# Performance work log

Hardware: AMD Instinct MI355X
Metric: run time of the kernel (lower is better)

## Reference

```python
import jax, jax.numpy as jnp
import numpy as np

# Kornia's fixed 5x5 pyramid (binomial) kernel used by build_pyramid/pyrdown
_PYR_K = np.array([[1, 4, 6, 4, 1],
                   [4, 16, 24, 16, 4],
                   [6, 24, 36, 24, 6],
                   [4, 16, 24, 16, 4],
                   [1, 4, 6, 4, 1]], dtype=np.float32) / 256.0


def _pyrdown(x):
    """kornia pyrdown: 5x5 binomial blur (reflect pad) + bilinear resize to (H//2, W//2)."""
    B, C, H, W = x.shape
    xp = jnp.pad(x, ((0, 0), (0, 0), (2, 2), (2, 2)), mode='reflect')
    k = jnp.broadcast_to(jnp.asarray(_PYR_K, x.dtype), (C, 1, 5, 5))  # depthwise
    y = jax.lax.conv_general_dilated(
        xp, k, window_strides=(1, 1), padding='VALID',
        feature_group_count=C, dimension_numbers=('NCHW', 'OIHW', 'NCHW'))
    # torch F.interpolate bilinear align_corners=False == jax resize bilinear, antialias off
    return jax.image.resize(y, (B, C, H // 2, W // 2), method='bilinear', antialias=False)


def _norm_pc(x):
    """Per-channel min-max normalization to [0,1] over spatial dims."""
    mx = jnp.max(x, axis=(2, 3), keepdims=True)
    mn = jnp.min(x, axis=(2, 3), keepdims=True)
    return (x - mn) / (mx - mn)


def _avg_local_max(x):
    """Mean of 16x16 tile maxima; torch loop range(0, H-16, 16) skips the last tile
    row/col, and with zero tiles the torch code yields nan_to_num(0/0) == 0."""
    B, C, H, W = x.shape
    s = 16
    ny = len(range(0, H - s, s))
    nx = len(range(0, W - s, s))
    if ny == 0 or nx == 0:
        return jnp.zeros((B, C, 1, 1), x.dtype)
    t = x[:, :, :ny * s, :nx * s].reshape(B, C, ny, s, nx, s)
    lmax = jnp.max(t, axis=(3, 5))           # [B,C,ny,nx]
    return jnp.mean(lmax, axis=(2, 3)).reshape(B, C, 1, 1)


def _sm_normalization(x):
    d = _norm_pc(x)
    lm = _avg_local_max(d)
    return d * (1.0 - lm) ** 2


def setup_inputs() -> dict:
    key = jax.random.key(0)
    x = jax.random.normal(key, (8, 3, 512, 512), dtype=jnp.float32)
    return {"x": x}


def reference(x):
    B, C, H, W = x.shape
    inp = _norm_pc(x)
    max_level = int(H).bit_length() - 1   # 9 for H=512
    u = max_level - 1

    # Gaussian pyramid of length max_level: [inp, pyrdown(inp), ...]
    pyr = [inp]
    for _ in range(max_level - 1):
        pyr.append(_pyrdown(pyr[-1]))

    acc = None
    for i in range(u - 1):
        h, w = pyr[i + 1].shape[2], pyr[i + 1].shape[3]
        up = jnp.repeat(jnp.repeat(pyr[i + 2], 2, axis=2), 2, axis=3)[:, :, :h, :w]
        d = jnp.abs(pyr[i + 1] - up)
        nd = jax.image.resize(_sm_normalization(d), (B, C, H, W),
                              method='bilinear', antialias=False)
        acc = nd if acc is None else acc + nd

    return jnp.mean(acc, axis=1)  # [B,H,W]
```

## Files before the change

kernel.cpp:

```cpp
#include <hip/hip_runtime.h>
#include <math.h>

#define NPLANES 24
#define FINF 3.402823466e38f

__host__ __device__ __forceinline__ int d_off(int li) {
    return 2097152 - (2097152 >> (2 * li));
}

__device__ __forceinline__ int refl(int v, int S) {
    if (v < 0) v = -v;
    if (v >= S) v = 2 * S - 2 - v;
    return v;
}

__device__ __forceinline__ void wminmax64(float& mn, float& mx) {
#pragma unroll
    for (int o = 32; o > 0; o >>= 1) {
        mn = fminf(mn, __shfl_xor(mn, o, 64));
        mx = fmaxf(mx, __shfl_xor(mx, o, 64));
    }
}
__device__ __forceinline__ float wsumx64(float v) {
#pragma unroll
    for (int o = 32; o > 0; o >>= 1) v += __shfl_xor(v, o, 64);
    return v;
}

__device__ __forceinline__ float stencil6(const float* s, int S, int i, int j) {
    const float w[6] = {1.f, 5.f, 10.f, 10.f, 5.f, 1.f};
    int rx[6];
#pragma unroll
    for (int b = 0; b < 6; ++b) rx[b] = refl(2 * j - 2 + b, S);
    float acc = 0.f;
#pragma unroll
    for (int a = 0; a < 6; ++a) {
        int ry = refl(2 * i - 2 + a, S);
        const float* rp = s + ry * S;
        float r = 0.f;
#pragma unroll
        for (int b = 0; b < 6; ++b) r += w[b] * rp[rx[b]];
        acc += w[a] * r;
    }
    return acc * (1.f / 1024.f);
}

template <int IS, bool HAS_D>
__global__ __launch_bounds__(256) void pyrdown_tiled(const float* __restrict__ in,
                                                     float* __restrict__ out,
                                                     float* __restrict__ dout,
                                                     float* __restrict__ tileMin,
                                                     float* __restrict__ tileMax) {
    constexpr int SO = IS / 2;
    constexpr int TO = 32;
    constexpr int TI = 2 * TO + 4;
    constexpr int TPA = SO / TO;
    __shared__ float sIn[TI * TI];
    __shared__ float sH[TI * TO];
    __shared__ float sOut[TO * TO];
    __shared__ float sD[HAS_D ? 64 * 65 : 1];
    __shared__ float rmn[HAS_D ? 256 : 1], rmx[HAS_D ? 256 : 1];

    const int tid = threadIdx.x;
    const int p = blockIdx.x / (TPA * TPA);
    const int t = blockIdx.x % (TPA * TPA);
    const int ty = t / TPA, tx = t % TPA;
    const int oy = ty * TO, ox = tx * TO;
    const int iy = 2 * oy - 2, ix = 2 * ox - 2;
    const float* ip = in + (size_t)p * IS * IS;

    for (int k = tid; k < TI * TI; k += 256) {
        int r = k / TI, c = k - r * TI;
        sIn[k] = ip[refl(iy + r, IS) * IS + refl(ix + c, IS)];
    }
    __syncthreads();

    for (int k = tid; k < TI * 8; k += 256) {
        int r = k >> 3, jq = k & 7;
        const float4* rp = (const float4*)(sIn + r * TI + 8 * jq);
        float4 v0 = rp[0], v1 = rp[1], v2 = rp[2];
        float4 o;
        o.x = v0.x + 5.f * v0.y + 10.f * v0.z + 10.f * v0.w + 5.f * v1.x + v1.y;
        o.y = v0.z + 5.f * v0.w + 10.f * v1.x + 10.f * v1.y + 5.f * v1.z + v1.w;
        o.z = v1.x + 5.f * v1.y + 10.f * v1.z + 10.f * v1.w + 5.f * v2.x + v2.y;
        o.w = v1.z + 5.f * v1.w + 10.f * v2.x + 10.f * v2.y + 5.f * v2.z + v2.w;
        *(float4*)(sH + r * TO + 4 * jq) = o;
    }
    __syncthreads();

    {
        int i = tid >> 3, jq = tid & 7;
        const float* base = sH + (2 * i) * TO + 4 * jq;
        float4 r0 = *(const float4*)(base);
        float4 r1 = *(const float4*)(base + TO);
        float4 r2 = *(const float4*)(base + 2 * TO);
        float4 r3 = *(const float4*)(base + 3 * TO);
        float4 r4 = *(const float4*)(base + 4 * TO);
        float4 r5 = *(const float4*)(base + 5 * TO);
        float4 o;
        o.x = (r0.x + 5.f * r1.x + 10.f * r2.x + 10.f * r3.x + 5.f * r4.x + r5.x) * (1.f / 1024.f);
        o.y = (r0.y + 5.f * r1.y + 10.f * r2.y + 10.f * r3.y + 5.f * r4.y + r5.y) * (1.f / 1024.f);
        o.z = (r0.z + 5.f * r1.z + 10.f * r2.z + 10.f * r3.z + 5.f * r4.z + r5.z) * (1.f / 1024.f);
        o.w = (r0.w + 5.f * r1.w + 10.f * r2.w + 10.f * r3.w + 5.f * r4.w + r5.w) * (1.f / 1024.f);
        *(float4*)(sOut + i * TO + 4 * jq) = o;
        *(float4*)(out + (size_t)p * SO * SO + (size_t)(oy + i) * SO + ox + 4 * jq) = o;
    }

    if (HAS_D) {
        __syncthreads();
        float* dp = dout + (size_t)p * IS * IS;
        for (int k = tid; k < 4096; k += 256) {
            int yy = k >> 6, xx = k & 63;
            float dv = fabsf(sIn[(yy + 2) * TI + xx + 2] - sOut[(yy >> 1) * TO + (xx >> 1)]);
            sD[yy * 65 + xx] = dv;
            dp[(size_t)(2 * oy + yy) * IS + 2 * ox + xx] = dv;
        }
        __syncthreads();
        int s = tid >> 4, r = tid & 15;
        int tr = s >> 2, tc = s & 3;
        const float* rowp = sD + (tr * 16 + r) * 65 + tc * 16;
        float mn = FINF, mx = -FINF;
#pragma unroll
        for (int c = 0; c < 16; ++c) {
            float v = rowp[c];
            mn = fminf(mn, v); mx = fmaxf(mx, v);
        }
        rmn[tid] = mn; rmx[tid] = mx;
        __syncthreads();
        for (int st = 8; st > 0; st >>= 1) {
            if (r < st) {
                rmn[tid] = fminf(rmn[tid], rmn[tid + st]);
                rmx[tid] = fmaxf(rmx[tid], rmx[tid + st]);
            }
            __syncthreads();
        }
        if (r == 0) {
            constexpr int TA = IS / 16;
            int gidx = p * TA * TA + (ty * 4 + tr) * TA + (tx * 4 + tc);
            tileMin[gidx] = rmn[tid];
            tileMax[gidx] = rmx[tid];
        }
    }
}

__global__ __launch_bounds__(1024) void fused_small_kernel(const float* __restrict__ pyr2,
                                                           float* __restrict__ dBase,
                                                           const float* __restrict__ tileMin,
                                                           const float* __restrict__ tileMax,
                                                           float* __restrict__ A,
                                                           float* __restrict__ B) {
    __shared__ float sP2[16384];
    __shared__ float sHbuf[8192];
    __shared__ float sP3[4096];
    float* sd2 = sHbuf;
    float* sp4 = sHbuf + 4096;
    float* sd3 = sHbuf + 5120;
    float* sp5 = sHbuf + 6144;
    float* sd4 = sHbuf + 6400;
    float* sp6 = sHbuf + 6656;
    float* sd5 = sHbuf + 6720;
    float* sp7 = sHbuf + 6784;
    float* sd6 = sHbuf + 6800;
    const int tid = threadIdx.x;
    const int p = blockIdx.x;

    {
        const float4* gp = (const float4*)(pyr2 + (size_t)p * 16384);
        float4* sv = (float4*)sP2;
        for (int k = tid; k < 4096; k += 1024) sv[k] = gp[k];
    }
    __syncthreads();
    for (int k = tid; k < 8192; k += 1024) {
        int r = k >> 6, c = k & 63;
        int b0 = 2 * c - 2;
        const float* rp = sP2 + r * 128;
        sHbuf[k] = rp[refl(b0, 128)] + 5.f * rp[refl(b0 + 1, 128)] + 10.f * rp[refl(b0 + 2, 128)] +
                   10.f * rp[refl(b0 + 3, 128)] + 5.f * rp[refl(b0 + 4, 128)] + rp[refl(b0 + 5, 128)];
    }
    __syncthreads();
    for (int k = tid; k < 4096; k += 1024) {
        int r3 = k >> 6, c = k & 63;
        int b0 = 2 * r3 - 2;
        float s = sHbuf[refl(b0, 128) * 64 + c] + 5.f * sHbuf[refl(b0 + 1, 128) * 64 + c] +
                  10.f * sHbuf[refl(b0 + 2, 128) * 64 + c] + 10.f * sHbuf[refl(b0 + 3, 128) * 64 + c] +
                  5.f * sHbuf[refl(b0 + 4, 128) * 64 + c] + sHbuf[refl(b0 + 5, 128) * 64 + c];
        sP3[k] = s * (1.f / 1024.f);
    }
    __syncthreads();
    {
        float4* d1g = (float4*)(dBase + d_off(1) + (size_t)p * 16384);
        float4* sv = (float4*)sP2;
        for (int k = tid; k < 4096; k += 1024) {
            int row = k >> 5, c4 = k & 31;
            float4 v = sv[k];
            float2 o = *(const float2*)(sP3 + (row >> 1) * 64 + 2 * c4);
            float4 dv;
            dv.x = fabsf(v.x - o.x);
            dv.y = fabsf(v.y - o.x);
            dv.z = fabsf(v.z - o.y);
            dv.w = fabsf(v.w - o.y);
            sv[k] = dv;
            d1g[k] = dv;
        }
    }
    __syncthreads();
    {
        float* d2g = dBase + d_off(2) + (size_t)p * 4096;
        int i = tid >> 5, j = tid & 31;
        float v = stencil6(sP3, 64, i, j);
        sp4[tid] = v;
#pragma unroll
        for (int di = 0; di < 2; ++di)
#pragma unroll
            for (int dj = 0; dj < 2; ++dj) {
                int y = 2 * i + di, x = 2 * j + dj;
                float dv = fabsf(sP3[y * 64 + x] - v);
                sd2[y * 64 + x] = dv;
                d2g[y * 64 + x] = dv;
            }
    }
    __syncthreads();

    const int wave = tid >> 6, lane = tid & 63;

    if (wave == 0) {
        float* d3g = dBase + d_off(3) + (size_t)p * 1024;
#pragma unroll
        for (int q = 0; q < 4; ++q) {
            int k = lane + 64 * q;
            int i = k >> 4, j = k & 15;
            float v = stencil6(sp4, 32, i, j);
            sp5[k] = v;
#pragma unroll
            for (int di = 0; di < 2; ++di)
#pragma unroll
                for (int dj = 0; dj < 2; ++dj) {
                    int y = 2 * i + di, x = 2 * j + dj;
                    float dv = fabsf(sp4[y * 32 + x] - v);
                    sd3[y * 32 + x] = dv;
                    d3g[y * 32 + x] = dv;
                }
        }
        {
            int i = lane >> 3, j = lane & 7;
            float v = stencil6(sp5, 16, i, j);
            sp6[lane] = v;
            float* d4g = dBase + d_off(4) + (size_t)p * 256;
#pragma unroll
            for (int di = 0; di < 2; ++di)
#pragma unroll
                for (int dj = 0; dj < 2; ++dj) {
                    int y = 2 * i + di, x = 2 * j + dj;
                    float dv = fabsf(sp5[y * 16 + x] - v);
                    sd4[y * 16 + x] = dv;
                    d4g[y * 16 + x] = dv;
                }
        }
        if (lane < 16) {
            int i = lane >> 2, j = lane & 3;
            float v = stencil6(sp6, 8, i, j);
            sp7[lane] = v;
            float* d5g = dBase + d_off(5) + (size_t)p * 64;
#pragma unroll
            for (int di = 0; di < 2; ++di)
#pragma unroll
                for (int dj = 0; dj < 2; ++dj) {
                    int y = 2 * i + di, x = 2 * j + dj;
                    float dv = fabsf(sp6[y * 8 + x] - v);
                    sd5[y * 8 + x] = dv;
                    d5g[y * 8 + x] = dv;
                }
        }
        if (lane < 4) {
            int i = lane >> 1, j = lane & 1;
            float v = stencil6(sp7, 4, i, j);
            float* d6g = dBase + d_off(6) + (size_t)p * 16;
#pragma unroll
            for (int di = 0; di < 2; ++di)
#pragma unroll
                for (int dj = 0; dj < 2; ++dj) {
                    int y = 2 * i + di, x = 2 * j + dj;
                    float dv = fabsf(sp7[y * 4 + x] - v);
                    sd6[y * 4 + x] = dv;
                    d6g[y * 4 + x] = dv;
                }
        }
    } else if (wave == 1) {
        const float4* sv = (const float4*)sP2;
        float mn = FINF, mx = -FINF;
        for (int k = lane; k < 4096; k += 64) {
            float4 v = sv[k];
            mn = fminf(mn, fminf(fminf(v.x, v.y), fminf(v.z, v.w)));
            mx = fmaxf(mx, fmaxf(fmaxf(v.x, v.y), fmaxf(v.z, v.w)));
        }
        wminmax64(mn, mx);
        float tmax = 0.f;
        if (lane < 49) {
            int tr = lane / 7, tc = lane % 7;
            const float4* base = (const float4*)(sP2 + (tr * 16) * 128 + tc * 16);
            float tm = -FINF;
            for (int r = 0; r < 16; ++r) {
#pragma unroll
                for (int c = 0; c < 4; ++c) {
                    float4 v = base[r * 32 + c];
                    tm = fmaxf(tm, fmaxf(fmaxf(v.x, v.y), fmaxf(v.z, v.w)));
                }
            }
            tmax = tm;
        }
        float sum = wsumx64(tmax);
        if (lane == 0) {
            float inv = 1.f / (mx - mn);
            float lm = (sum * (1.f / 49.f) - mn) * inv;
            float g = (1.f - lm) * (1.f - lm);
            A[1 * NPLANES + p] = g * inv;
            B[1 * NPLANES + p] = -mn * g * inv;
        }
    } else if (wave == 2) {
        float mn = FINF, mx = -FINF, su = 0.f;
#pragma unroll
        for (int q = 0; q < 4; ++q) {
            int t = lane + 64 * q;
            float tmn = tileMin[p * 256 + t];
            float tmx = tileMax[p * 256 + t];
            mn = fminf(mn, tmn);
            mx = fmaxf(mx, tmx);
            if ((t >> 4) < 15 && (t & 15) < 15) su += tmx;
        }
        wminmax64(mn, mx);
        float sum = wsumx64(su);
        if (lane == 0) {
            float inv = 1.f / (mx - mn);
            float lm = (sum * (1.f / 225.f) - mn) * inv;
            float g = (1.f - lm) * (1.f - lm);
            A[0 * NPLANES + p] = g * inv;
            B[0 * NPLANES + p] = -mn * g * inv;
        }
    }
    __syncthreads();

    if (wave == 0) {
        const float4* sv = (const float4*)sd2;
        float mn = FINF, mx = -FINF;
#pragma unroll
        for (int q = 0; q < 16; ++q) {
            float4 v = sv[lane + 64 * q];
            mn = fminf(mn, fminf(fminf(v.x, v.y), fminf(v.z, v.w)));
            mx = fmaxf(mx, fmaxf(fmaxf(v.x, v.y), fmaxf(v.z, v.w)));
        }
        wminmax64(mn, mx);
        float tmax = -FINF;
        if (lane < 36) {
            int t = lane >> 2, r4 = lane & 3;
            int tr = t / 3, tc = t % 3;
#pragma unroll
            for (int rr = 0; rr < 4; ++rr) {
                const float4* base = (const float4*)(sd2 + (16 * tr + 4 * r4 + rr) * 64 + 16 * tc);
#pragma unroll
                for (int c = 0; c < 4; ++c) {
                    float4 v = base[c];
                    tmax = fmaxf(tmax, fmaxf(fmaxf(v.x, v.y), fmaxf(v.z, v.w)));
                }
            }
        }
        tmax = fmaxf(tmax, __shfl_xor(tmax, 1, 64));
        tmax = fmaxf(tmax, __shfl_xor(tmax, 2, 64));
        float val = ((lane & 3) == 0 && lane < 36) ? tmax : 0.f;
        float s = wsumx64(val);
        if (lane == 0) {
            float inv = 1.f / (mx - mn);
            float lm = (s * (1.f / 9.f) - mn) * inv;
            float g = (1.f - lm) * (1.f - lm);
            A[2 * NPLANES + p] = g * inv;
            B[2 * NPLANES + p] = -mn * g * inv;
        }
    } else if (wave == 1) {
        const float4* sv = (const float4*)sd3;
        float mn = FINF, mx = -FINF;
#pragma unroll
        for (int q = 0; q < 4; ++q) {
            float4 v = sv[lane + 64 * q];
            mn = fminf(mn, fminf(fminf(v.x, v.y), fminf(v.z, v.w)));
            mx = fmaxf(mx, fmaxf(fmaxf(v.x, v.y), fmaxf(v.z, v.w)));
        }
        wminmax64(mn, mx);
        float4 e4 = sv[(lane >> 2) * 8 + (lane & 3)];
        float e = fmaxf(fmaxf(e4.x, e4.y), fmaxf(e4.z, e4.w));
        float tn = e, tm = e;
        wminmax64(tn, tm);
        if (lane == 0) {
            float inv = 1.f / (mx - mn);
            float lm = (tm - mn) * inv;
            float g = (1.f - lm) * (1.f - lm);
            A[3 * NPLANES + p] = g * inv;
            B[3 * NPLANES + p] = -mn * g * inv;
        }
    } else if (wave == 2) {
        float4 v = ((const float4*)sd4)[lane];
        float mn = fminf(fminf(v.x, v.y), fminf(v.z, v.w));
        float mx = fmaxf(fmaxf(v.x, v.y), fmaxf(v.z, v.w));
        wminmax64(mn, mx);
        if (lane == 0) {
            float inv = 1.f / (mx - mn);
            A[4 * NPLANES + p] = inv; B[4 * NPLANES + p] = -mn * inv;
        }
    } else if (wave == 3) {
        float v = sd5[lane];
        float mn = v, mx = v;
        wminmax64(mn, mx);
        if (lane == 0) {
            float inv = 1.f / (mx - mn);
            A[5 * NPLANES + p] = inv; B[5 * NPLANES + p] = -mn * inv;
        }
    } else if (wave == 4) {
        float v = (lane < 16) ? sd6[lane] : sd6[0];
        float mn = v, mx = v;
        wminmax64(mn, mx);
        if (lane == 0) {
            float inv = 1.f / (mx - mn);
            A[6 * NPLANES + p] = inv; B[6 * NPLANES + p] = -mn * inv;
        }
    }
}

__global__ __launch_bounds__(256) void final_kernel(const float* __restrict__ dBase,
                                                    const float* __restrict__ A,
                                                    const float* __restrict__ Bc,
                                                    float* __restrict__ out) {
    __shared__ float patch[1700];
    __shared__ float sBtot;
    const int tid = threadIdx.x;
    const int b = blockIdx.x >> 6;
    const int tile = blockIdx.x & 63;
    const int yb = (tile >> 3) << 6;
    const int xb = (tile & 7) << 6;

    if (tid == 0) {
        float s = 0.f;
        for (int k = 0; k < 7; ++k)
            for (int c = 0; c < 3; ++c) s += Bc[k * NPLANES + b * 3 + c];
        sBtot = s;
    }

    const int dims[7] = {34, 18, 10, 6, 4, 3, 3};
    const int lofs[7] = {0, 1156, 1480, 1580, 1616, 1632, 1641};
    int baseY[7], baseX[7];
#pragma unroll
    for (int li = 0; li < 7; ++li) {
        const int S = 256 >> li;
        const float s = 1.f / (float)(2 << li);
        baseY[li] = (int)floorf((yb + 0.5f) * s - 0.5f);
        baseX[li] = (int)floorf((xb + 0.5f) * s - 0.5f);
        const int dim = dims[li];
        const int n = dim * dim;
        const float* d0p = dBase + d_off(li) + (size_t)(b * 3) * S * S;
        const float* d1p = d0p + S * S;
        const float* d2p = d1p + S * S;
        const float A0 = A[li * NPLANES + b * 3 + 0];
        const float A1 = A[li * NPLANES + b * 3 + 1];
        const float A2 = A[li * NPLANES + b * 3 + 2];
        for (int k = tid; k < n; k += 256) {
            int r = k / dim, c = k - r * dim;
            int sr = min(max(baseY[li] + r, 0), S - 1);
            int sc = min(max(baseX[li] + c, 0), S - 1);
            int si = sr * S + sc;
            patch[lofs[li] + k] = A0 * d0p[si] + A1 * d1p[si] + A2 * d2p[si];
        }
    }
    __syncthreads();

    const int ty = tid >> 4, tx = tid & 15;
    const int gy0 = yb + (ty << 2), gx0 = xb + (tx << 2);
    float acc[4][4];
#pragma unroll
    for (int i = 0; i < 4; ++i)
#pragma unroll
        for (int j = 0; j < 4; ++j) acc[i][j] = 0.f;

    {
        const int dim = 34;
        float wy[4], wx[4];
        int ry[4], cx[4];
#pragma unroll
        for (int k = 0; k < 4; ++k) {
            float fy = (gy0 + k + 0.5f) * 0.5f - 0.5f;
            float fl = floorf(fy);
            wy[k] = fy - fl; ry[k] = (int)fl - baseY[0];
            float fx = (gx0 + k + 0.5f) * 0.5f - 0.5f;
            fl = floorf(fx);
            wx[k] = fx - fl; cx[k] = (int)fl - baseX[0];
        }
        const int r0 = ry[0], c0 = cx[0];
        const float* pp = patch + r0 * dim + c0;
        float P[4][4];
#pragma unroll
        for (int r = 0; r < 4; ++r)
#pragma unroll
            for (int c = 0; c < 4; ++c) P[r][c] = pp[r * dim + c];
        float h[4][4];
#pragma unroll
        for (int j = 0; j < 4; ++j) {
            int dx = cx[j] - c0;
#pragma unroll
            for (int r = 0; r < 4; ++r) {
                float a = dx == 0 ? P[r][0] : (dx == 1 ? P[r][1] : P[r][2]);
                float bb = dx == 0 ? P[r][1] : (dx == 1 ? P[r][2] : P[r][3]);
                h[r][j] = a + wx[j] * (bb - a);
            }
        }
#pragma unroll
        for (int i = 0; i < 4; ++i) {
            int dy = ry[i] - r0;
#pragma unroll
            for (int j = 0; j < 4; ++j) {
                float h0 = dy == 0 ? h[0][j] : (dy == 1 ? h[1][j] : h[2][j]);
                float h1 = dy == 0 ? h[1][j] : (dy == 1 ? h[2][j] : h[3][j]);
                acc[i][j] += h0 + wy[i] * (h1 - h0);
            }
        }
    }
#pragma unroll
    for (int li = 1; li < 7; ++li) {
        const int dim = dims[li];
        const float* P0 = patch + lofs[li];
        const float s = 1.f / (float)(2 << li);
        float wy[4], wx[4];
        int ry[4], cx[4];
#pragma unroll
        for (int k = 0; k < 4; ++k) {
            float fy = (gy0 + k + 0.5f) * s - 0.5f;
            float fl = floorf(fy);
            wy[k] = fy - fl; ry[k] = (int)fl - baseY[li];
            float fx = (gx0 + k + 0.5f) * s - 0.5f;
            fl = floorf(fx);
            wx[k] = fx - fl; cx[k] = (int)fl - baseX[li];
        }
        const int r0 = ry[0], c0 = cx[0];
        const float* pp = P0 + r0 * dim + c0;
        float P[3][3];
#pragma unroll
        for (int r = 0; r < 3; ++r)
#pragma unroll
            for (int c = 0; c < 3; ++c) P[r][c] = pp[r * dim + c];
        float h[3][4];
#pragma unroll
        for (int j = 0; j < 4; ++j) {
            int dx = cx[j] - c0;
#pragma unroll
            for (int r = 0; r < 3; ++r) {
                float a = dx == 0 ? P[r][0] : P[r][1];
                float bb = dx == 0 ? P[r][1] : P[r][2];
                h[r][j] = a + wx[j] * (bb - a);
            }
        }
#pragma unroll
        for (int i = 0; i < 4; ++i) {
            int dy = ry[i] - r0;
#pragma unroll
            for (int j = 0; j < 4; ++j) {
                float h0 = dy == 0 ? h[0][j] : h[1][j];
                float h1 = dy == 0 ? h[1][j] : h[2][j];
                acc[i][j] += h0 + wy[i] * (h1 - h0);
            }
        }
    }

    const float bt = sBtot;
    float* op = out + ((size_t)b * 512 + gy0) * 512 + gx0;
#pragma unroll
    for (int i = 0; i < 4; ++i) {
        float4 v;
        v.x = (acc[i][0] + bt) * (1.f / 3.f);
        v.y = (acc[i][1] + bt) * (1.f / 3.f);
        v.z = (acc[i][2] + bt) * (1.f / 3.f);
        v.w = (acc[i][3] + bt) * (1.f / 3.f);
        *(float4*)(op + (size_t)i * 512) = v;
    }
}

extern "C" void kernel_launch(void* const* d_in, const int* in_sizes, int n_in,
                              void* d_out, int out_size, void* d_ws, size_t ws_size,
                              hipStream_t stream) {
    (void)in_sizes; (void)n_in; (void)out_size; (void)ws_size;
    const float* x = (const float*)d_in[0];
    float* ws = (float*)d_ws;
    float* out = (float*)d_out;

    float* pyr1 = ws;
    float* pyr2 = ws + 1572864;
    float* dBase = ws + 1966080;
    float* tileMin = ws + 4063104;
    float* tileMax = ws + 4069248;
    float* A = ws + 4075392;
    float* Bc = ws + 4075560;

    pyrdown_tiled<512, false><<<NPLANES * 64, 256, 0, stream>>>(x, pyr1, nullptr, nullptr, nullptr);
    pyrdown_tiled<256, true><<<NPLANES * 16, 256, 0, stream>>>(pyr1, pyr2, dBase + d_off(0), tileMin, tileMax);
    fused_small_kernel<<<NPLANES, 1024, 0, stream>>>(pyr2, dBase, tileMin, tileMax, A, Bc);
    final_kernel<<<8 * 64, 256, 0, stream>>>(dBase, A, Bc, out);
}
```

Measured before the change: 109.4 us.

## Fuse pyramid levels 2 and 3 into one tiled kernel, moving level-1 work out of single-block kernel

A new tiled kernel, spread over many blocks, computes pyr2 and pyr3 together from pyr1 using a larger halo. It writes the level-0 and level-1 difference maps and their per-16x16-tile min/max. The per-plane fused_small_kernel, which runs only 24 blocks, no longer loads the 128x128 pyr2 plane, blurs it, or scans it for min/max. It now reads pyr3 and the precomputed tile statistics instead. This shrinks the serial, low-parallelism stage and removes the pyr2 round trip through global memory. In exchange, overlapping halos are recomputed in each block.

```diff
diff --git a/kernel.cpp b/kernel.cpp
--- a/kernel.cpp
+++ b/kernel.cpp
@@ -26,6 +26,13 @@
     for (int o = 32; o > 0; o >>= 1) v += __shfl_xor(v, o, 64);
     return v;
 }
+__device__ __forceinline__ void wminmax16(float& mn, float& mx) {
+#pragma unroll
+    for (int o = 8; o > 0; o >>= 1) {
+        mn = fminf(mn, __shfl_xor(mn, o, 16));
+        mx = fmaxf(mx, __shfl_xor(mx, o, 16));
+    }
+}
 
 __device__ __forceinline__ float stencil6(const float* s, int S, int i, int j) {
     const float w[6] = {1.f, 5.f, 10.f, 10.f, 5.f, 1.f};
@@ -45,22 +52,11 @@
     return acc * (1.f / 1024.f);
 }
 
-template <int IS, bool HAS_D>
-__global__ __launch_bounds__(256) void pyrdown_tiled(const float* __restrict__ in,
-                                                     float* __restrict__ out,
-                                                     float* __restrict__ dout,
-                                                     float* __restrict__ tileMin,
-                                                     float* __restrict__ tileMax) {
-    constexpr int SO = IS / 2;
-    constexpr int TO = 32;
-    constexpr int TI = 2 * TO + 4;
-    constexpr int TPA = SO / TO;
+__global__ __launch_bounds__(256) void pyrdown_l1(const float* __restrict__ in,
+                                                  float* __restrict__ out) {
+    constexpr int IS = 512, SO = 256, TO = 32, TI = 68, TPA = 8;
     __shared__ float sIn[TI * TI];
     __shared__ float sH[TI * TO];
-    __shared__ float sOut[TO * TO];
-    __shared__ float sD[HAS_D ? 64 * 65 : 1];
-    __shared__ float rmn[HAS_D ? 256 : 1], rmx[HAS_D ? 256 : 1];
-
     const int tid = threadIdx.x;
     const int p = blockIdx.x / (TPA * TPA);
     const int t = blockIdx.x % (TPA * TPA);
@@ -74,7 +70,6 @@
         sIn[k] = ip[refl(iy + r, IS) * IS + refl(ix + c, IS)];
     }
     __syncthreads();
-
     for (int k = tid; k < TI * 8; k += 256) {
         int r = k >> 3, jq = k & 7;
         const float4* rp = (const float4*)(sIn + r * TI + 8 * jq);
@@ -87,7 +82,6 @@
         *(float4*)(sH + r * TO + 4 * jq) = o;
     }
     __syncthreads();
-
     {
         int i = tid >> 3, jq = tid & 7;
         const float* base = sH + (2 * i) * TO + 4 * jq;
@@ -102,107 +96,149 @@
         o.y = (r0.y + 5.f * r1.y + 10.f * r2.y + 10.f * r3.y + 5.f * r4.y + r5.y) * (1.f / 1024.f);
         o.z = (r0.z + 5.f * r1.z + 10.f * r2.z + 10.f * r3.z + 5.f * r4.z + r5.z) * (1.f / 1024.f);
         o.w = (r0.w + 5.f * r1.w + 10.f * r2.w + 10.f * r3.w + 5.f * r4.w + r5.w) * (1.f / 1024.f);
-        *(float4*)(sOut + i * TO + 4 * jq) = o;
         *(float4*)(out + (size_t)p * SO * SO + (size_t)(oy + i) * SO + ox + 4 * jq) = o;
     }
-
-    if (HAS_D) {
-        __syncthreads();
-        float* dp = dout + (size_t)p * IS * IS;
-        for (int k = tid; k < 4096; k += 256) {
-            int yy = k >> 6, xx = k & 63;
-            float dv = fabsf(sIn[(yy + 2) * TI + xx + 2] - sOut[(yy >> 1) * TO + (xx >> 1)]);
-            sD[yy * 65 + xx] = dv;
-            dp[(size_t)(2 * oy + yy) * IS + 2 * ox + xx] = dv;
-        }
-        __syncthreads();
-        int s = tid >> 4, r = tid & 15;
-        int tr = s >> 2, tc = s & 3;
-        const float* rowp = sD + (tr * 16 + r) * 65 + tc * 16;
+}
+
+__global__ __launch_bounds__(256) void pyrdown23(const float* __restrict__ pyr1,
+                                                 float* __restrict__ pyr3,
+                                                 float* __restrict__ dBase,
+                                                 float* __restrict__ tmin0,
+                                                 float* __restrict__ tmax0,
+                                                 float* __restrict__ tmin1,
+                                                 float* __restrict__ tmax1) {
+    __shared__ float sIn[5776];
+    __shared__ float sH1[2736];
+    __shared__ float sP2[1296];
+    __shared__ float sH2[576];
+    __shared__ float sP3t[256];
+    const int tid = threadIdx.x;
+    const int p = blockIdx.x >> 4;
+    const int t = blockIdx.x & 15;
+    const int t3y = t >> 2, t3x = t & 3;
+    const int oy3 = t3y * 16, ox3 = t3x * 16;
+    const int oy2 = 2 * oy3, ox2 = 2 * ox3;
+    const int py0 = oy2 - 2, px0 = ox2 - 2;
+    const int iy0 = 2 * py0 - 2, ix0 = 2 * px0 - 2;
+    const float* ip = pyr1 + (size_t)p * 65536;
+
+    for (int k = tid; k < 5776; k += 256) {
+        int r = k / 76, c = k - r * 76;
+        sIn[k] = ip[refl(iy0 + r, 256) * 256 + refl(ix0 + c, 256)];
+    }
+    __syncthreads();
+    for (int k = tid; k < 2736; k += 256) {
+        int r = k / 36, c2 = k - r * 36;
+        const float* rp = sIn + r * 76 + 2 * c2;
+        sH1[k] = rp[0] + 5.f * rp[1] + 10.f * rp[2] + 10.f * rp[3] + 5.f * rp[4] + rp[5];
+    }
+    __syncthreads();
+    for (int k = tid; k < 1296; k += 256) {
+        int r2 = k / 36, c2 = k - r2 * 36;
+        const float* cp = sH1 + 2 * r2 * 36 + c2;
+        sP2[k] = (cp[0] + 5.f * cp[36] + 10.f * cp[72] + 10.f * cp[108] +
+                  5.f * cp[144] + cp[180]) * (1.f / 1024.f);
+    }
+    __syncthreads();
+    for (int k = tid; k < 576; k += 256) {
+        int r2 = k >> 4, c3 = k & 15;
+        int gb = 2 * (ox3 + c3) - 2;
+        const float* rp = sP2 + r2 * 36;
+        sH2[k] = rp[refl(gb, 128) - px0] + 5.f * rp[refl(gb + 1, 128) - px0] +
+                 10.f * rp[refl(gb + 2, 128) - px0] + 10.f * rp[refl(gb + 3, 128) - px0] +
+                 5.f * rp[refl(gb + 4, 128) - px0] + rp[refl(gb + 5, 128) - px0];
+    }
+    __syncthreads();
+    {
+        int i3 = tid >> 4, c3 = tid & 15;
+        int gb = 2 * (oy3 + i3) - 2;
+        float s = sH2[(refl(gb, 128) - py0) * 16 + c3] +
+                  5.f * sH2[(refl(gb + 1, 128) - py0) * 16 + c3] +
+                  10.f * sH2[(refl(gb + 2, 128) - py0) * 16 + c3] +
+                  10.f * sH2[(refl(gb + 3, 128) - py0) * 16 + c3] +
+                  5.f * sH2[(refl(gb + 4, 128) - py0) * 16 + c3] +
+                  sH2[(refl(gb + 5, 128) - py0) * 16 + c3];
+        float v = s * (1.f / 1024.f);
+        sP3t[tid] = v;
+        pyr3[(size_t)p * 4096 + (size_t)(oy3 + i3) * 64 + ox3 + c3] = v;
+    }
+    __syncthreads();
+    {
+        float* d0g = dBase + (size_t)p * 65536;
+        int ti = tid >> 4, si = tid & 15;
+        int tr = ti >> 2, tc = ti & 3;
+        int y0 = tr * 16 + (si >> 2) * 4, x0 = tc * 16 + (si & 3) * 4;
         float mn = FINF, mx = -FINF;
 #pragma unroll
-        for (int c = 0; c < 16; ++c) {
-            float v = rowp[c];
-            mn = fminf(mn, v); mx = fmaxf(mx, v);
-        }
-        rmn[tid] = mn; rmx[tid] = mx;
-        __syncthreads();
-        for (int st = 8; st > 0; st >>= 1) {
-            if (r < st) {
-                rmn[tid] = fminf(rmn[tid], rmn[tid + st]);
-                rmx[tid] = fmaxf(rmx[tid], rmx[tid + st]);
-            }
-            __syncthreads();
-        }
-        if (r == 0) {
-            constexpr int TA = IS / 16;
-            int gidx = p * TA * TA + (ty * 4 + tr) * TA + (tx * 4 + tc);
-            tileMin[gidx] = rmn[tid];
-            tileMax[gidx] = rmx[tid];
-        }
-    }
-}
-
-__global__ __launch_bounds__(1024) void fused_small_kernel(const float* __restrict__ pyr2,
+        for (int r = 0; r < 4; ++r) {
+            int y = y0 + r;
+            const float* srow = sIn + (y + 6) * 76 + x0 + 6;
+            const float* prow = sP2 + ((y >> 1) + 2) * 36 + 2 + (x0 >> 1);
+            float e0 = prow[0], e1 = prow[1];
+            float4 dv;
+            dv.x = fabsf(srow[0] - e0);
+            dv.y = fabsf(srow[1] - e0);
+            dv.z = fabsf(srow[2] - e1);
+            dv.w = fabsf(srow[3] - e1);
+            *(float4*)(d0g + (size_t)(4 * oy3 + y) * 256 + 4 * ox3 + x0) = dv;
+            mn = fminf(mn, fminf(fminf(dv.x, dv.y), fminf(dv.z, dv.w)));
+            mx = fmaxf(mx, fmaxf(fmaxf(dv.x, dv.y), fmaxf(dv.z, dv.w)));
+        }
+        wminmax16(mn, mx);
+        if (si == 0) {
+            int g0 = p * 256 + (t3y * 4 + tr) * 16 + (t3x * 4 + tc);
+            tmin0[g0] = mn;
+            tmax0[g0] = mx;
+        }
+    }
+    if (tid < 64) {
+        float* d1g = dBase + d_off(1) + (size_t)p * 16384;
+        int ti = tid >> 4, si = tid & 15;
+        int tr = ti >> 1, tc = ti & 1;
+        int y0 = tr * 16 + (si >> 2) * 4, x0 = tc * 16 + (si & 3) * 4;
+        float mn = FINF, mx = -FINF;
+#pragma unroll
+        for (int r = 0; r < 4; ++r) {
+            int y = y0 + r;
+            const float* prow = sP2 + (y + 2) * 36 + 2 + x0;
+            const float* qrow = sP3t + (y >> 1) * 16 + (x0 >> 1);
+            float e0 = qrow[0], e1 = qrow[1];
+            float4 dv;
+            dv.x = fabsf(prow[0] - e0);
+            dv.y = fabsf(prow[1] - e0);
+            dv.z = fabsf(prow[2] - e1);
+            dv.w = fabsf(prow[3] - e1);
+            *(float4*)(d1g + (size_t)(oy2 + y) * 128 + ox2 + x0) = dv;
+            mn = fminf(mn, fminf(fminf(dv.x, dv.y), fminf(dv.z, dv.w)));
+            mx = fmaxf(mx, fmaxf(fmaxf(dv.x, dv.y), fmaxf(dv.z, dv.w)));
+        }
+        wminmax16(mn, mx);
+        if (si == 0) {
+            int g1 = p * 64 + (t3y * 2 + tr) * 8 + (t3x * 2 + tc);
+            tmin1[g1] = mn;
+            tmax1[g1] = mx;
+        }
+    }
+}
+
+__global__ __launch_bounds__(1024) void fused_small_kernel(const float* __restrict__ pyr3,
                                                            float* __restrict__ dBase,
-                                                           const float* __restrict__ tileMin,
-                                                           const float* __restrict__ tileMax,
+                                                           const float* __restrict__ tmin0,
+                                                           const float* __restrict__ tmax0,
+                                                           const float* __restrict__ tmin1,
+                                                           const float* __restrict__ tmax1,
                                                            float* __restrict__ A,
                                                            float* __restrict__ B) {
-    __shared__ float sP2[16384];
-    __shared__ float sHbuf[8192];
     __shared__ float sP3[4096];
-    float* sd2 = sHbuf;
-    float* sp4 = sHbuf + 4096;
-    float* sd3 = sHbuf + 5120;
-    float* sp5 = sHbuf + 6144;
-    float* sd4 = sHbuf + 6400;
-    float* sp6 = sHbuf + 6656;
-    float* sd5 = sHbuf + 6720;
-    float* sp7 = sHbuf + 6784;
-    float* sd6 = sHbuf + 6800;
+    __shared__ float sd2[4096];
+    __shared__ float sp4[1024], sd3[1024];
+    __shared__ float sp5[256], sd4[256];
+    __shared__ float sp6[64], sd5[64];
+    __shared__ float sp7[16], sd6[16];
     const int tid = threadIdx.x;
     const int p = blockIdx.x;
 
-    {
-        const float4* gp = (const float4*)(pyr2 + (size_t)p * 16384);
-        float4* sv = (float4*)sP2;
-        for (int k = tid; k < 4096; k += 1024) sv[k] = gp[k];
-    }
-    __syncthreads();
-    for (int k = tid; k < 8192; k += 1024) {
-        int r = k >> 6, c = k & 63;
-        int b0 = 2 * c - 2;
-        const float* rp = sP2 + r * 128;
-        sHbuf[k] = rp[refl(b0, 128)] + 5.f * rp[refl(b0 + 1, 128)] + 10.f * rp[refl(b0 + 2, 128)] +
-                   10.f * rp[refl(b0 + 3, 128)] + 5.f * rp[refl(b0 + 4, 128)] + rp[refl(b0 + 5, 128)];
-    }
-    __syncthreads();
-    for (int k = tid; k < 4096; k += 1024) {
-        int r3 = k >> 6, c = k & 63;
-        int b0 = 2 * r3 - 2;
-        float s = sHbuf[refl(b0, 128) * 64 + c] + 5.f * sHbuf[refl(b0 + 1, 128) * 64 + c] +
-                  10.f * sHbuf[refl(b0 + 2, 128) * 64 + c] + 10.f * sHbuf[refl(b0 + 3, 128) * 64 + c] +
-                  5.f * sHbuf[refl(b0 + 4, 128) * 64 + c] + sHbuf[refl(b0 + 5, 128) * 64 + c];
-        sP3[k] = s * (1.f / 1024.f);
-    }
-    __syncthreads();
-    {
-        float4* d1g = (float4*)(dBase + d_off(1) + (size_t)p * 16384);
-        float4* sv = (float4*)sP2;
-        for (int k = tid; k < 4096; k += 1024) {
-            int row = k >> 5, c4 = k & 31;
-            float4 v = sv[k];
-            float2 o = *(const float2*)(sP3 + (row >> 1) * 64 + 2 * c4);
-            float4 dv;
-            dv.x = fabsf(v.x - o.x);
-            dv.y = fabsf(v.y - o.x);
-            dv.z = fabsf(v.z - o.y);
-            dv.w = fabsf(v.w - o.y);
-            sv[k] = dv;
-            d1g[k] = dv;
-        }
-    }
+    if (tid < 1024) ((float4*)sP3)[tid] = ((const float4*)(pyr3 + (size_t)p * 4096))[tid];
     __syncthreads();
     {
         float* d2g = dBase + d_off(2) + (size_t)p * 4096;
@@ -286,29 +322,12 @@
                 }
         }
     } else if (wave == 1) {
-        const float4* sv = (const float4*)sP2;
-        float mn = FINF, mx = -FINF;
-        for (int k = lane; k < 4096; k += 64) {
-            float4 v = sv[k];
-            mn = fminf(mn, fminf(fminf(v.x, v.y), fminf(v.z, v.w)));
-            mx = fmaxf(mx, fmaxf(fmaxf(v.x, v.y), fmaxf(v.z, v.w)));
-        }
+        float tmn = tmin1[p * 64 + lane];
+        float tmx = tmax1[p * 64 + lane];
+        float mn = tmn, mx = tmx;
         wminmax64(mn, mx);
-        float tmax = 0.f;
-        if (lane < 49) {
-            int tr = lane / 7, tc = lane % 7;
-            const float4* base = (const float4*)(sP2 + (tr * 16) * 128 + tc * 16);
-            float tm = -FINF;
-            for (int r = 0; r < 16; ++r) {
-#pragma unroll
-                for (int c = 0; c < 4; ++c) {
-                    float4 v = base[r * 32 + c];
-                    tm = fmaxf(tm, fmaxf(fmaxf(v.x, v.y), fmaxf(v.z, v.w)));
-                }
-            }
-            tmax = tm;
-        }
-        float sum = wsumx64(tmax);
+        float su = ((lane >> 3) < 7 && (lane & 7) < 7) ? tmx : 0.f;
+        float sum = wsumx64(su);
         if (lane == 0) {
             float inv = 1.f / (mx - mn);
             float lm = (sum * (1.f / 49.f) - mn) * inv;
@@ -321,8 +340,8 @@
 #pragma unroll
         for (int q = 0; q < 4; ++q) {
             int t = lane + 64 * q;
-            float tmn = tileMin[p * 256 + t];
-            float tmx = tileMax[p * 256 + t];
+            float tmn = tmin0[p * 256 + t];
+            float tmx = tmax0[p * 256 + t];
             mn = fminf(mn, tmn);
             mx = fmaxf(mx, tmx);
             if ((t >> 4) < 15 && (t & 15) < 15) su += tmx;
@@ -587,15 +606,17 @@
     float* out = (float*)d_out;
 
     float* pyr1 = ws;
-    float* pyr2 = ws + 1572864;
-    float* dBase = ws + 1966080;
-    float* tileMin = ws + 4063104;
-    float* tileMax = ws + 4069248;
-    float* A = ws + 4075392;
-    float* Bc = ws + 4075560;
-
-    pyrdown_tiled<512, false><<<NPLANES * 64, 256, 0, stream>>>(x, pyr1, nullptr, nullptr, nullptr);
-    pyrdown_tiled<256, true><<<NPLANES * 16, 256, 0, stream>>>(pyr1, pyr2, dBase + d_off(0), tileMin, tileMax);
-    fused_small_kernel<<<NPLANES, 1024, 0, stream>>>(pyr2, dBase, tileMin, tileMax, A, Bc);
+    float* pyr3 = ws + 1572864;
+    float* dBase = ws + 1671168;
+    float* tmin0 = ws + 3768192;
+    float* tmax0 = ws + 3774336;
+    float* tmin1 = ws + 3780480;
+    float* tmax1 = ws + 3782016;
+    float* A = ws + 3783552;
+    float* Bc = ws + 3783720;
+
+    pyrdown_l1<<<NPLANES * 64, 256, 0, stream>>>(x, pyr1);
+    pyrdown23<<<NPLANES * 16, 256, 0, stream>>>(pyr1, pyr3, dBase, tmin0, tmax0, tmin1, tmax1);
+    fused_small_kernel<<<NPLANES, 1024, 0, stream>>>(pyr3, dBase, tmin0, tmax0, tmin1, tmax1, A, Bc);
     final_kernel<<<8 * 64, 256, 0, stream>>>(dBase, A, Bc, out);
 }
```

After: 103.9 us. -5.0%, faster.
